# Kernel optimization log

Hardware: AMD Instinct MI355X
Metric: run time of the kernel (lower is better)

Reference implementation:

```python
import itertools
import jax, jax.numpy as jnp
import numpy as np

L, B, K, C = 2048, 64, 4, 128
LOSS_SUBSET = 0.25


def setup_inputs() -> dict:
    key = jax.random.key(0)
    ks = jax.random.split(key, 8)
    in_time = jnp.cumsum(jax.random.uniform(ks[0], (L, B)), axis=0)
    in_amount = jax.random.normal(ks[1], (L, B))
    in_mcc = jax.random.randint(ks[2], (L, B), 0, C)
    out_time = jax.random.uniform(ks[3], (L, B, K))
    out_amount = jax.random.normal(ks[4], (L, B, K))
    out_logits = jax.random.normal(ks[5], (L, B, K, C))
    presence = jax.random.normal(ks[6], (L, B, K))
    lengths = jax.random.randint(ks[7], (B,), L // 2 + K + 1, L + 1)
    # --- get_loss_indices (randomness hoisted out of forward) ---
    n_idx = min(max(int(round(L * LOSS_SUBSET)), 1), L)  # 512
    mask = (jnp.arange(L)[None, :] + K) < lengths[:, None]  # (B, L)
    weights = jax.random.uniform(jax.random.fold_in(key, 123), (B, L)) * mask
    _, idx = jax.lax.top_k(weights, n_idx)  # (B, I)
    idx = jnp.sort(idx, axis=1)
    subset_lengths = jnp.sum((idx + K) < lengths[:, None], axis=1)  # (B,)
    indices = idx.T  # (I, B)
    return {
        "in_time": in_time, "in_amount": in_amount, "in_mcc": in_mcc,
        "out_time": out_time, "out_amount": out_amount, "out_logits": out_logits,
        "presence": presence, "lengths": lengths,
        "indices": indices, "subset_lengths": subset_lengths,
    }


def _windows(x):
    # (L, B, ...) -> (L, B, K+1, ...): rolling window of next K steps + current
    return jnp.stack([jnp.roll(x, -i, axis=0) for i in range(K + 1)], axis=2)


def _select(x, indices):
    # gather along dim 0 with per-batch indices (I, B)
    idx = indices.reshape(indices.shape + (1,) * (x.ndim - 2))
    return jnp.take_along_axis(x, idx, axis=0)


def _loss_core(in_time, in_amount, in_mcc, out_time, out_amount, out_logits,
               presence, indices, subset_lengths):
    T = K
    I = indices.shape[0]
    # structured windows over inputs
    tw = _select(_windows(in_time), indices)      # (I, B, K+1)
    aw = _select(_windows(in_amount), indices)    # (I, B, K+1)
    cw = _select(_windows(in_mcc), indices)       # (I, B, K+1)
    ot = _select(out_time, indices)               # (I, B, K)
    oa = _select(out_amount, indices)             # (I, B, K)
    ol = _select(out_logits, indices)             # (I, B, K, C)
    ps = _select(presence, indices)               # (I, B, K)
    # valid mask: indices are sorted, first subset_lengths[b] positions valid
    m = (jnp.arange(I)[:, None] < subset_lengths[None, :]).reshape(-1)  # (N,)
    N = I * B
    V = jnp.sum(m.astype(jnp.float32))
    # categorical cross-entropy cost (N, K, T)
    logp = jax.nn.log_softmax(ol.reshape(N, K, C), axis=-1)
    true_c = cw.reshape(N, K + 1)[:, 1:]  # (N, T)
    ce = -jnp.take_along_axis(logp[:, :, None, :], true_c[:, None, :, None], axis=3)[..., 0]
    # time L1 cost: deltas relative to current step
    t_full = tw.reshape(N, K + 1)
    t_true = t_full[:, 1:] - t_full[:, :1]  # (N, T)
    l1_t = jnp.abs(ot.reshape(N, K)[:, :, None] - t_true[:, None, :])
    # amount L1 cost
    a_true = aw.reshape(N, K + 1)[:, 1:]
    l1_a = jnp.abs(oa.reshape(N, K)[:, :, None] - a_true[:, None, :])
    # presence cost
    pres = ps.reshape(N, K)
    cost = ce + l1_t + l1_a - pres[:, :, None]  # (N, K, T), all weights = 1
    # exact batched linear assignment via permutation enumeration (K = T = 4)
    perms = jnp.asarray(np.array(list(itertools.permutations(range(K))), dtype=np.int32))  # (P, K)
    perm_cost = cost[:, jnp.arange(K)[None, :], perms].sum(-1)  # (N, P)
    assign = perms[jnp.argmin(perm_cost, axis=1)]  # (N, K)
    gathered = jnp.take_along_axis(cost, assign[:, :, None], axis=2)[..., 0].sum(1)  # (N,)
    loss = jnp.sum(gathered * m)
    leftover = jnp.sum(-jax.nn.log_sigmoid(-pres) * m[:, None])
    return (loss + leftover) / V


def reference(in_time, in_amount, in_mcc, out_time, out_amount, out_logits,
              presence, lengths, indices, subset_lengths):
    return _loss_core(in_time, in_amount, in_mcc, out_time, out_amount,
                      out_logits, presence, indices, subset_lengths)
```

## Files before the change

kernel.cpp:

```cpp
#include <hip/hip_runtime.h>

#define LL 2048
#define BB 64
#define KT 4
#define CC 128
#define II 512
#define NPOS (II * BB)

__global__ __launch_bounds__(256) void detpp_main(
    const float* __restrict__ in_time,
    const float* __restrict__ in_amount,
    const int*   __restrict__ in_mcc,
    const float* __restrict__ out_time,
    const float* __restrict__ out_amount,
    const float* __restrict__ out_logits,
    const float* __restrict__ presence,
    const int*   __restrict__ indices,
    const int*   __restrict__ subset_lengths,
    float* __restrict__ partials)
{
    const int blk = blockIdx.x;
    const int i   = blk >> 6;
    const int b   = blk & 63;
    const int tid = threadIdx.x;

    __shared__ float s_tw[KT + 1], s_aw[KT + 1];
    __shared__ int   s_cw[KT + 1];
    __shared__ float s_ot[KT], s_oa[KT], s_ps[KT];
    __shared__ float s_cost[KT][KT];
    __shared__ int   s_idx, s_valid;

    if (tid == 0) {
        s_idx   = indices[blk];
        s_valid = (i < subset_lengths[b]) ? 1 : 0;
    }
    __syncthreads();

    if (!s_valid) {
        if (tid == 0) partials[blk] = 0.0f;
        return;
    }
    const int idx = s_idx;

    if (tid < KT + 1) {
        int row = idx + tid;
        if (row >= LL) row -= LL;
        s_tw[tid] = in_time[row * BB + b];
        s_aw[tid] = in_amount[row * BB + b];
        s_cw[tid] = in_mcc[row * BB + b];
    } else if (tid >= 64 && tid < 64 + KT) {
        const int k = tid - 64;
        const size_t base = ((size_t)idx * BB + b) * KT + k;
        s_ot[k] = out_time[base];
        s_oa[k] = out_amount[base];
        s_ps[k] = presence[base];
    }
    __syncthreads();

    const int wave = tid >> 6;
    const int lane = tid & 63;

    const size_t lbase = (((size_t)idx * BB + b) * KT + wave) * CC;
    const float2 v = *reinterpret_cast<const float2*>(out_logits + lbase + lane * 2);

    float mx = fmaxf(v.x, v.y);
    #pragma unroll
    for (int m = 32; m >= 1; m >>= 1) mx = fmaxf(mx, __shfl_xor(mx, m));
    float se = __expf(v.x - mx) + __expf(v.y - mx);
    #pragma unroll
    for (int m = 32; m >= 1; m >>= 1) se += __shfl_xor(se, m);
    const float lse = mx + logf(se);

    if (lane < KT) {
        const int t = lane;
        const float ol_true = out_logits[lbase + s_cw[t + 1]];
        const float ce  = lse - ol_true;
        const float l1t = fabsf(s_ot[wave] - (s_tw[t + 1] - s_tw[0]));
        const float l1a = fabsf(s_oa[wave] - s_aw[t + 1]);
        s_cost[wave][t] = ce + l1t + l1a - s_ps[wave];
    }
    __syncthreads();

    if (tid == 0) {
        float c[KT][KT];
        #pragma unroll
        for (int k = 0; k < KT; k++)
            #pragma unroll
            for (int t = 0; t < KT; t++) c[k][t] = s_cost[k][t];

        const signed char P[24][4] = {
            {0,1,2,3},{0,1,3,2},{0,2,1,3},{0,2,3,1},{0,3,1,2},{0,3,2,1},
            {1,0,2,3},{1,0,3,2},{1,2,0,3},{1,2,3,0},{1,3,0,2},{1,3,2,0},
            {2,0,1,3},{2,0,3,1},{2,1,0,3},{2,1,3,0},{2,3,0,1},{2,3,1,0},
            {3,0,1,2},{3,0,2,1},{3,1,0,2},{3,1,2,0},{3,2,0,1},{3,2,1,0}};
        float best = 3.4e38f;
        #pragma unroll
        for (int p = 0; p < 24; p++) {
            const float s = c[0][P[p][0]] + c[1][P[p][1]] +
                            c[2][P[p][2]] + c[3][P[p][3]];
            best = fminf(best, s);
        }

        float leftover = 0.0f;
        #pragma unroll
        for (int k = 0; k < KT; k++) {
            const float x = s_ps[k];
            leftover += fmaxf(x, 0.0f) + log1pf(__expf(-fabsf(x)));
        }
        partials[blk] = best + leftover;
    }
}

__global__ __launch_bounds__(1024) void detpp_finish(
    const float* __restrict__ partials,
    const int*   __restrict__ subset_lengths,
    float* __restrict__ out)
{
    const int tid = threadIdx.x;
    float s = 0.0f;
    for (int j = tid; j < NPOS; j += 1024) s += partials[j];
    #pragma unroll
    for (int m = 32; m >= 1; m >>= 1) s += __shfl_xor(s, m);

    __shared__ float red[16];
    const int wave = tid >> 6;
    const int lane = tid & 63;
    if (lane == 0) red[wave] = s;
    __syncthreads();

    if (tid == 0) {
        float tot = 0.0f;
        #pragma unroll
        for (int w = 0; w < 16; w++) tot += red[w];
        int V = 0;
        for (int bb = 0; bb < BB; bb++) V += subset_lengths[bb];
        out[0] = tot / (float)V;
    }
}

extern "C" void kernel_launch(void* const* d_in, const int* in_sizes, int n_in,
                              void* d_out, int out_size, void* d_ws, size_t ws_size,
                              hipStream_t stream) {
    const float* in_time        = (const float*)d_in[0];
    const float* in_amount      = (const float*)d_in[1];
    const int*   in_mcc         = (const int*)  d_in[2];
    const float* out_time       = (const float*)d_in[3];
    const float* out_amount     = (const float*)d_in[4];
    const float* out_logits     = (const float*)d_in[5];
    const float* presence       = (const float*)d_in[6];
    const int*   indices        = (const int*)  d_in[8];
    const int*   subset_lengths = (const int*)  d_in[9];

    float* partials = (float*)d_ws;

    detpp_main<<<NPOS, 256, 0, stream>>>(
        in_time, in_amount, in_mcc, out_time, out_amount, out_logits,
        presence, indices, subset_lengths, partials);

    detpp_finish<<<1, 1024, 0, stream>>>(partials, subset_lengths, (float*)d_out);
}
```

Before: 377.8 us.

## Process one position per wavefront using shuffles instead of shared-memory block syncs

```diff
diff --git a/kernel.cpp b/kernel.cpp
--- a/kernel.cpp
+++ b/kernel.cpp
@@ -19,96 +19,105 @@
     const int*   __restrict__ subset_lengths,
     float* __restrict__ partials)
 {
-    const int blk = blockIdx.x;
-    const int i   = blk >> 6;
-    const int b   = blk & 63;
-    const int tid = threadIdx.x;
+    const int lane = threadIdx.x & 63;
+    const int wv   = threadIdx.x >> 6;
+    const int p    = (blockIdx.x << 2) | wv;
+    const int i    = p >> 6;
+    const int b    = p & 63;
 
-    __shared__ float s_tw[KT + 1], s_aw[KT + 1];
-    __shared__ int   s_cw[KT + 1];
-    __shared__ float s_ot[KT], s_oa[KT], s_ps[KT];
-    __shared__ float s_cost[KT][KT];
-    __shared__ int   s_idx, s_valid;
-
-    if (tid == 0) {
-        s_idx   = indices[blk];
-        s_valid = (i < subset_lengths[b]) ? 1 : 0;
-    }
-    __syncthreads();
-
-    if (!s_valid) {
-        if (tid == 0) partials[blk] = 0.0f;
+    if (i >= subset_lengths[b]) {
+        if (lane == 0) partials[p] = 0.0f;
         return;
     }
-    const int idx = s_idx;
 
-    if (tid < KT + 1) {
-        int row = idx + tid;
-        if (row >= LL) row -= LL;
-        s_tw[tid] = in_time[row * BB + b];
-        s_aw[tid] = in_amount[row * BB + b];
-        s_cw[tid] = in_mcc[row * BB + b];
-    } else if (tid >= 64 && tid < 64 + KT) {
-        const int k = tid - 64;
-        const size_t base = ((size_t)idx * BB + b) * KT + k;
-        s_ot[k] = out_time[base];
-        s_oa[k] = out_amount[base];
-        s_ps[k] = presence[base];
+    const int idx = indices[p];
+    const size_t obase = ((size_t)idx * BB + b) * KT;
+    const float* __restrict__ lrow = out_logits + obase * CC;
+
+    float tval = 0.0f, aval = 0.0f, otv = 0.0f, oav = 0.0f, psv = 0.0f;
+    int   cval = 0;
+    if (lane < 5)                      tval = in_time  [(((idx + lane)      & (LL - 1)) << 6) + b];
+    else if (lane >= 8  && lane < 13)  aval = in_amount[(((idx + lane - 8)  & (LL - 1)) << 6) + b];
+    else if (lane >= 16 && lane < 21)  cval = in_mcc   [(((idx + lane - 16) & (LL - 1)) << 6) + b];
+    else if (lane >= 24 && lane < 28)  otv = out_time  [obase + lane - 24];
+    else if (lane >= 32 && lane < 36)  oav = out_amount[obase + lane - 32];
+    else if (lane >= 40 && lane < 44)  psv = presence  [obase + lane - 40];
+
+    const float2* l2 = reinterpret_cast<const float2*>(lrow) + lane;
+    const float2 v0 = l2[0 * (CC / 2)];
+    const float2 v1 = l2[1 * (CC / 2)];
+    const float2 v2 = l2[2 * (CC / 2)];
+    const float2 v3 = l2[3 * (CC / 2)];
+
+#define LSE(vx, out)                                                      \
+    {                                                                     \
+        float mx = fmaxf(vx.x, vx.y);                                     \
+        _Pragma("unroll")                                                 \
+        for (int m = 32; m >= 1; m >>= 1) mx = fmaxf(mx, __shfl_xor(mx, m)); \
+        float se = __expf(vx.x - mx) + __expf(vx.y - mx);                 \
+        _Pragma("unroll")                                                 \
+        for (int m = 32; m >= 1; m >>= 1) se += __shfl_xor(se, m);        \
+        out = mx + logf(se);                                              \
     }
-    __syncthreads();
+    float lse0, lse1, lse2, lse3;
+    LSE(v0, lse0) LSE(v1, lse1) LSE(v2, lse2) LSE(v3, lse3)
+#undef LSE
 
-    const int wave = tid >> 6;
-    const int lane = tid & 63;
+    const int k = lane >> 2;
+    const int t = lane & 3;
+    const int ct = __shfl(cval, 16 + 1 + t);
+    float ol = 0.0f;
+    if (lane < 16) ol = lrow[k * CC + ct];
+    const float lsek = (k == 0) ? lse0 : (k == 1) ? lse1 : (k == 2) ? lse2 : lse3;
+    const float tw0  = __shfl(tval, 0);
+    const float twt1 = __shfl(tval, 1 + t);
+    const float awt1 = __shfl(aval, 9 + t);
+    const float ot_k = __shfl(otv, 24 + k);
+    const float oa_k = __shfl(oav, 32 + k);
+    const float ps_k = __shfl(psv, 40 + k);
+    const float cmy = (lsek - ol)
+                    + fabsf(ot_k - (twt1 - tw0))
+                    + fabsf(oa_k - awt1)
+                    - ps_k;
 
-    const size_t lbase = (((size_t)idx * BB + b) * KT + wave) * CC;
-    const float2 v = *reinterpret_cast<const float2*>(out_logits + lbase + lane * 2);
+    const float c0  = __shfl(cmy, 0),  c1  = __shfl(cmy, 1),  c2  = __shfl(cmy, 2),  c3  = __shfl(cmy, 3);
+    const float c4  = __shfl(cmy, 4),  c5  = __shfl(cmy, 5),  c6  = __shfl(cmy, 6),  c7  = __shfl(cmy, 7);
+    const float c8  = __shfl(cmy, 8),  c9  = __shfl(cmy, 9),  c10 = __shfl(cmy, 10), c11 = __shfl(cmy, 11);
+    const float c12 = __shfl(cmy, 12), c13 = __shfl(cmy, 13), c14 = __shfl(cmy, 14), c15 = __shfl(cmy, 15);
 
-    float mx = fmaxf(v.x, v.y);
-    #pragma unroll
-    for (int m = 32; m >= 1; m >>= 1) mx = fmaxf(mx, __shfl_xor(mx, m));
-    float se = __expf(v.x - mx) + __expf(v.y - mx);
-    #pragma unroll
-    for (int m = 32; m >= 1; m >>= 1) se += __shfl_xor(se, m);
-    const float lse = mx + logf(se);
+    float best = c0 + c5 + c10 + c15;
+    best = fminf(best, c0 + c5 + c11 + c14);
+    best = fminf(best, c0 + c6 + c9  + c15);
+    best = fminf(best, c0 + c6 + c11 + c13);
+    best = fminf(best, c0 + c7 + c9  + c14);
+    best = fminf(best, c0 + c7 + c10 + c13);
+    best = fminf(best, c1 + c4 + c10 + c15);
+    best = fminf(best, c1 + c4 + c11 + c14);
+    best = fminf(best, c1 + c6 + c8  + c15);
+    best = fminf(best, c1 + c6 + c11 + c12);
+    best = fminf(best, c1 + c7 + c8  + c14);
+    best = fminf(best, c1 + c7 + c10 + c12);
+    best = fminf(best, c2 + c4 + c9  + c15);
+    best = fminf(best, c2 + c4 + c11 + c13);
+    best = fminf(best, c2 + c5 + c8  + c15);
+    best = fminf(best, c2 + c5 + c11 + c12);
+    best = fminf(best, c2 + c7 + c8  + c13);
+    best = fminf(best, c2 + c7 + c9  + c12);
+    best = fminf(best, c3 + c4 + c9  + c14);
+    best = fminf(best, c3 + c4 + c10 + c13);
+    best = fminf(best, c3 + c5 + c8  + c14);
+    best = fminf(best, c3 + c5 + c10 + c12);
+    best = fminf(best, c3 + c6 + c8  + c13);
+    best = fminf(best, c3 + c6 + c9  + c12);
 
-    if (lane < KT) {
-        const int t = lane;
-        const float ol_true = out_logits[lbase + s_cw[t + 1]];
-        const float ce  = lse - ol_true;
-        const float l1t = fabsf(s_ot[wave] - (s_tw[t + 1] - s_tw[0]));
-        const float l1a = fabsf(s_oa[wave] - s_aw[t + 1]);
-        s_cost[wave][t] = ce + l1t + l1a - s_ps[wave];
+    float leftover = 0.0f;
+#pragma unroll
+    for (int kk = 0; kk < KT; kk++) {
+        const float x = __shfl(psv, 40 + kk);
+        leftover += fmaxf(x, 0.0f) + log1pf(__expf(-fabsf(x)));
     }
-    __syncthreads();
 
-    if (tid == 0) {
-        float c[KT][KT];
-        #pragma unroll
-        for (int k = 0; k < KT; k++)
-            #pragma unroll
-            for (int t = 0; t < KT; t++) c[k][t] = s_cost[k][t];
-
-        const signed char P[24][4] = {
-            {0,1,2,3},{0,1,3,2},{0,2,1,3},{0,2,3,1},{0,3,1,2},{0,3,2,1},
-            {1,0,2,3},{1,0,3,2},{1,2,0,3},{1,2,3,0},{1,3,0,2},{1,3,2,0},
-            {2,0,1,3},{2,0,3,1},{2,1,0,3},{2,1,3,0},{2,3,0,1},{2,3,1,0},
-            {3,0,1,2},{3,0,2,1},{3,1,0,2},{3,1,2,0},{3,2,0,1},{3,2,1,0}};
-        float best = 3.4e38f;
-        #pragma unroll
-        for (int p = 0; p < 24; p++) {
-            const float s = c[0][P[p][0]] + c[1][P[p][1]] +
-                            c[2][P[p][2]] + c[3][P[p][3]];
-            best = fminf(best, s);
-        }
-
-        float leftover = 0.0f;
-        #pragma unroll
-        for (int k = 0; k < KT; k++) {
-            const float x = s_ps[k];
-            leftover += fmaxf(x, 0.0f) + log1pf(__expf(-fabsf(x)));
-        }
-        partials[blk] = best + leftover;
-    }
+    if (lane == 0) partials[p] = best + leftover;
 }
 
 __global__ __launch_bounds__(1024) void detpp_finish(
@@ -118,8 +127,9 @@
 {
     const int tid = threadIdx.x;
     float s = 0.0f;
+#pragma unroll 8
     for (int j = tid; j < NPOS; j += 1024) s += partials[j];
-    #pragma unroll
+#pragma unroll
     for (int m = 32; m >= 1; m >>= 1) s += __shfl_xor(s, m);
 
     __shared__ float red[16];
@@ -130,7 +140,7 @@
 
     if (tid == 0) {
         float tot = 0.0f;
-        #pragma unroll
+#pragma unroll
         for (int w = 0; w < 16; w++) tot += red[w];
         int V = 0;
         for (int bb = 0; bb < BB; bb++) V += subset_lengths[bb];
@@ -153,7 +163,7 @@
 
     float* partials = (float*)d_ws;
 
-    detpp_main<<<NPOS, 256, 0, stream>>>(
+    detpp_main<<<NPOS / 4, 256, 0, stream>>>(
         in_time, in_amount, in_mcc, out_time, out_amount, out_logits,
         presence, indices, subset_lengths, partials);
 
```

Result: faster. 356.3 us (-5.7%).
